# Optimization experiments

Measured on AMD Instinct MI355X. Metric: run time of the kernel, lower is better.

Reference implementation:

```python
import jax, jax.numpy as jnp
import numpy as np

B, L, D, K = 8, 256, 256, 64  # batch, slots, n_input, attn_dimension


def setup_inputs() -> dict:
    key = jax.random.key(0)
    k1, k2, k3 = jax.random.split(key, 3)
    inputs = jax.random.normal(k1, (B, L, D), dtype=jnp.float32)
    # torch.nn.Linear weights are [out_features, in_features]; scale to avoid tanh saturation
    W1 = jax.random.normal(k2, (K, 2 * D), dtype=jnp.float32) * (1.0 / np.sqrt(2 * D))
    W2 = jax.random.normal(k3, (1, K), dtype=jnp.float32) * (1.0 / np.sqrt(K))
    return {"inputs": inputs, "W1": W1, "W2": W2}


def reference(inputs, W1, W2):
    # CONCAT branch of SlotAttention:
    #   score[b,i,j] = W2 @ tanh(W1 @ concat(inputs[b,i], inputs[b,j]))
    # Split W1 into the halves acting on the i-part and j-part of the concat
    # (identical math, avoids materializing the [B,L,L,2D] concat tensor).
    d = inputs.shape[-1]
    W1i, W1j = W1[:, :d], W1[:, d:]
    qi = jnp.einsum('bld,kd->blk', inputs, W1i)          # [B,L,K]
    kj = jnp.einsum('bld,kd->blk', inputs, W1j)          # [B,L,K]
    h = jnp.tanh(qi[:, :, None, :] + kj[:, None, :, :])  # [B,L,L,K]
    scores = jnp.einsum('bijk,k->bij', h, W2[0])         # [B,L,L]
    attn = jax.nn.softmax(scores, axis=2)                # softmax over j
    context = jnp.einsum('bij,bjd->bid', attn, inputs)   # [B,L,D]
    return jnp.concatenate([inputs, context], axis=2)    # [B,L,2D]
```

## Files before the change

### kernel.cpp

```cpp
#include <hip/hip_runtime.h>


#define Bn 8
#define Ln 256
#define Dn 256
#define Kn 64
#define ROWS (Bn*Ln)
#define IPB 4

__global__ __launch_bounds__(128) void proj_kernel(
    const float* __restrict__ X,
    const float* __restrict__ W1,
    float* __restrict__ QK)
{
    __shared__ float Xs[4 * 256];
    const int tid = threadIdx.x;
    const int r0 = blockIdx.x * 4;

    const float4* Xg4 = (const float4*)(X + r0 * Dn);
    float4* Xs4 = (float4*)Xs;
    #pragma unroll
    for (int idx = tid; idx < 256; idx += 128) Xs4[idx] = Xg4[idx];
    __syncthreads();

    const int k = tid & 63, half = tid >> 6;
    const float4* Wrow = (const float4*)(W1 + k * (2 * Dn) + half * Dn);
    float acc[4] = {0, 0, 0, 0};
    #pragma unroll 8
    for (int d4 = 0; d4 < 64; ++d4) {
        float4 w = Wrow[d4];
        #pragma unroll
        for (int r = 0; r < 4; ++r) {
            float4 x = ((const float4*)(Xs + r * Dn))[d4];
            float a = acc[r];
            a = fmaf(w.x, x.x, a);
            a = fmaf(w.y, x.y, a);
            a = fmaf(w.z, x.z, a);
            a = fmaf(w.w, x.w, a);
            acc[r] = a;
        }
    }
    #pragma unroll
    for (int r = 0; r < 4; ++r)
        QK[(r0 + r) * 128 + tid] = __expf(2.0f * acc[r]);
}

__global__ __launch_bounds__(256) void attn_kernel(
    const float* __restrict__ X,
    const float* __restrict__ QK,
    const float* __restrict__ W2,
    float* __restrict__ out)
{
    __shared__ float eq_s[IPB * Kn];
    __shared__ float w2_s[Kn];
    __shared__ float S[Ln * IPB];
    __shared__ float4 red[4 * IPB * 64];

    const int tid = threadIdx.x;
    const int b  = blockIdx.x / (Ln / IPB);
    const int i0 = (blockIdx.x % (Ln / IPB)) * IPB;

    if (tid < Kn) w2_s[tid] = W2[tid];
    {
        int ii = tid >> 6, kk = tid & 63;
        eq_s[ii * Kn + kk] = QK[(b * Ln + i0 + ii) * 128 + kk];
    }

    float ekr[Kn];
    const float4* kj4 = (const float4*)(QK + (b * Ln + tid) * 128 + 64);
    #pragma unroll
    for (int q = 0; q < 16; ++q) {
        float4 v = kj4[q];
        ekr[q * 4 + 0] = v.x; ekr[q * 4 + 1] = v.y;
        ekr[q * 4 + 2] = v.z; ekr[q * 4 + 3] = v.w;
    }
    __syncthreads();

    float s[IPB] = {0, 0, 0, 0};
    const float4* w4  = (const float4*)w2_s;
    const float4* q4a = (const float4*)(eq_s);
    const float4* q4b = (const float4*)(eq_s + Kn);
    const float4* q4c = (const float4*)(eq_s + 2 * Kn);
    const float4* q4d = (const float4*)(eq_s + 3 * Kn);
    #pragma unroll
    for (int k4 = 0; k4 < 16; ++k4) {
        float4 w  = w4[k4];
        float4 q0 = q4a[k4], q1 = q4b[k4], q2 = q4c[k4], q3 = q4d[k4];
        #pragma unroll
        for (int c = 0; c < 4; ++c) {
            float ek = ekr[k4 * 4 + c];
            float wk = (c == 0) ? w.x : (c == 1) ? w.y : (c == 2) ? w.z : w.w;
            float e0 = (c == 0) ? q0.x : (c == 1) ? q0.y : (c == 2) ? q0.z : q0.w;
            float e1 = (c == 0) ? q1.x : (c == 1) ? q1.y : (c == 2) ? q1.z : q1.w;
            float e2 = (c == 0) ? q2.x : (c == 1) ? q2.y : (c == 2) ? q2.z : q2.w;
            float e3 = (c == 0) ? q3.x : (c == 1) ? q3.y : (c == 2) ? q3.z : q3.w;
            s[0] = fmaf(wk, __builtin_amdgcn_rcpf(fmaf(e0, ek, 1.0f)), s[0]);
            s[1] = fmaf(wk, __builtin_amdgcn_rcpf(fmaf(e1, ek, 1.0f)), s[1]);
            s[2] = fmaf(wk, __builtin_amdgcn_rcpf(fmaf(e2, ek, 1.0f)), s[2]);
            s[3] = fmaf(wk, __builtin_amdgcn_rcpf(fmaf(e3, ek, 1.0f)), s[3]);
        }
    }
    ((float4*)S)[tid] = make_float4(s[0], s[1], s[2], s[3]);
    __syncthreads();

    {
        const int wv = tid >> 6, lane = tid & 63;
        float e0 = __expf(-2.0f * S[(lane      ) * IPB + wv]);
        float e1 = __expf(-2.0f * S[(lane +  64) * IPB + wv]);
        float e2 = __expf(-2.0f * S[(lane + 128) * IPB + wv]);
        float e3 = __expf(-2.0f * S[(lane + 192) * IPB + wv]);
        float sum = (e0 + e1) + (e2 + e3);
        #pragma unroll
        for (int off = 32; off > 0; off >>= 1)
            sum += __shfl_xor(sum, off);
        float inv = 1.0f / sum;
        S[(lane      ) * IPB + wv] = e0 * inv;
        S[(lane +  64) * IPB + wv] = e1 * inv;
        S[(lane + 128) * IPB + wv] = e2 * inv;
        S[(lane + 192) * IPB + wv] = e3 * inv;
    }
    __syncthreads();

    {
        const int wv = tid >> 6, lane = tid & 63;
        float4 acc0 = {0,0,0,0}, acc1 = {0,0,0,0}, acc2 = {0,0,0,0}, acc3 = {0,0,0,0};
        const float4* Xb4 = (const float4*)(X + b * Ln * Dn);
        const float4* S4  = (const float4*)S;
        const int jbase = wv * 64;
        #pragma unroll 8
        for (int jj = 0; jj < 64; ++jj) {
            int j = jbase + jj;
            float4 at = S4[j];
            float4 x  = Xb4[j * 64 + lane];
            acc0.x = fmaf(at.x, x.x, acc0.x); acc0.y = fmaf(at.x, x.y, acc0.y);
            acc0.z = fmaf(at.x, x.z, acc0.z); acc0.w = fmaf(at.x, x.w, acc0.w);
            acc1.x = fmaf(at.y, x.x, acc1.x); acc1.y = fmaf(at.y, x.y, acc1.y);
            acc1.z = fmaf(at.y, x.z, acc1.z); acc1.w = fmaf(at.y, x.w, acc1.w);
            acc2.x = fmaf(at.z, x.x, acc2.x); acc2.y = fmaf(at.z, x.y, acc2.y);
            acc2.z = fmaf(at.z, x.z, acc2.z); acc2.w = fmaf(at.z, x.w, acc2.w);
            acc3.x = fmaf(at.w, x.x, acc3.x); acc3.y = fmaf(at.w, x.y, acc3.y);
            acc3.z = fmaf(at.w, x.z, acc3.z); acc3.w = fmaf(at.w, x.w, acc3.w);
        }
        red[(wv * IPB + 0) * 64 + lane] = acc0;
        red[(wv * IPB + 1) * 64 + lane] = acc1;
        red[(wv * IPB + 2) * 64 + lane] = acc2;
        red[(wv * IPB + 3) * 64 + lane] = acc3;
    }
    __syncthreads();

    {
        const int i = tid >> 6, q = tid & 63;
        float4 p0 = red[(0 * IPB + i) * 64 + q];
        float4 p1 = red[(1 * IPB + i) * 64 + q];
        float4 p2 = red[(2 * IPB + i) * 64 + q];
        float4 p3 = red[(3 * IPB + i) * 64 + q];
        float4 c;
        c.x = (p0.x + p1.x) + (p2.x + p3.x);
        c.y = (p0.y + p1.y) + (p2.y + p3.y);
        c.z = (p0.z + p1.z) + (p2.z + p3.z);
        c.w = (p0.w + p1.w) + (p2.w + p3.w);
        const int row = b * Ln + i0 + i;
        float4 xcopy = ((const float4*)(X + row * Dn))[q];
        ((float4*)(out + row * 2 * Dn))[q]      = xcopy;
        ((float4*)(out + row * 2 * Dn + Dn))[q] = c;
    }
}

extern "C" void kernel_launch(void* const* d_in, const int* in_sizes, int n_in,
                              void* d_out, int out_size, void* d_ws, size_t ws_size,
                              hipStream_t stream) {
    const float* X  = (const float*)d_in[0];
    const float* W1 = (const float*)d_in[1];
    const float* W2 = (const float*)d_in[2];
    float* out = (float*)d_out;
    float* QK  = (float*)d_ws;

    proj_kernel<<<ROWS / 4, 128, 0, stream>>>(X, W1, QK);
    attn_kernel<<<ROWS / IPB, 256, 0, stream>>>(X, QK, W2, out);
}
```

Measured before the change: 79.68 us.

## Fuse projection and attention into one cooperative kernel with grid sync

Merges the projection and attention kernels into a single cooperative launch of 512 blocks that use a grid-wide barrier between phases. The query-side exp values stay in shared memory and only the key side goes to the workspace. The X rows are reused from shared memory for the output copy. This removes a kernel launch and the gap between the two kernels, at the cost of a grid sync and the requirement that all 512 blocks be resident at once; the old two-kernel path is kept as a fallback if the cooperative launch fails.

```diff
diff --git a/kernel.cpp b/kernel.cpp
--- a/kernel.cpp
+++ b/kernel.cpp
@@ -1,4 +1,7 @@
 #include <hip/hip_runtime.h>
+#include <hip/hip_cooperative_groups.h>
+
+namespace cg = cooperative_groups;
 
 
 #define Bn 8
@@ -8,96 +11,109 @@
 #define ROWS (Bn*Ln)
 #define IPB 4
 
-__global__ __launch_bounds__(128) void proj_kernel(
+__global__ __launch_bounds__(256, 2) void fused_kernel(
     const float* __restrict__ X,
     const float* __restrict__ W1,
-    float* __restrict__ QK)
-{
-    __shared__ float Xs[4 * 256];
-    const int tid = threadIdx.x;
-    const int r0 = blockIdx.x * 4;
-
-    const float4* Xg4 = (const float4*)(X + r0 * Dn);
-    float4* Xs4 = (float4*)Xs;
-    #pragma unroll
-    for (int idx = tid; idx < 256; idx += 128) Xs4[idx] = Xg4[idx];
-    __syncthreads();
-
-    const int k = tid & 63, half = tid >> 6;
-    const float4* Wrow = (const float4*)(W1 + k * (2 * Dn) + half * Dn);
-    float acc[4] = {0, 0, 0, 0};
-    #pragma unroll 8
-    for (int d4 = 0; d4 < 64; ++d4) {
-        float4 w = Wrow[d4];
-        #pragma unroll
-        for (int r = 0; r < 4; ++r) {
-            float4 x = ((const float4*)(Xs + r * Dn))[d4];
-            float a = acc[r];
-            a = fmaf(w.x, x.x, a);
-            a = fmaf(w.y, x.y, a);
-            a = fmaf(w.z, x.z, a);
-            a = fmaf(w.w, x.w, a);
-            acc[r] = a;
-        }
-    }
-    #pragma unroll
-    for (int r = 0; r < 4; ++r)
-        QK[(r0 + r) * 128 + tid] = __expf(2.0f * acc[r]);
-}
-
-__global__ __launch_bounds__(256) void attn_kernel(
-    const float* __restrict__ X,
-    const float* __restrict__ QK,
     const float* __restrict__ W2,
+    float* __restrict__ QKek,
     float* __restrict__ out)
 {
+    __shared__ float Xs[IPB * Dn];
     __shared__ float eq_s[IPB * Kn];
     __shared__ float w2_s[Kn];
+    __shared__ float pr[128 * 4];
     __shared__ float S[Ln * IPB];
     __shared__ float4 red[4 * IPB * 64];
 
     const int tid = threadIdx.x;
-    const int b  = blockIdx.x / (Ln / IPB);
-    const int i0 = (blockIdx.x % (Ln / IPB)) * IPB;
-
+    const int blk = blockIdx.x;
+    const int r0  = blk * IPB;
+    const int b   = blk >> 6;
+
+    ((float4*)Xs)[tid] = ((const float4*)(X + r0 * Dn))[tid];
     if (tid < Kn) w2_s[tid] = W2[tid];
-    {
-        int ii = tid >> 6, kk = tid & 63;
-        eq_s[ii * Kn + kk] = QK[(b * Ln + i0 + ii) * 128 + kk];
-    }
+    __syncthreads();
+
+    {
+        const int c    = tid & 127;
+        const int dh   = tid >> 7;
+        const int k    = c & 63;
+        const int half = c >> 6;
+        const float4* Wrow = (const float4*)(W1 + k * (2 * Dn) + half * Dn + dh * (Dn / 2));
+        const float4* x0p = (const float4*)(Xs + 0 * Dn + dh * (Dn / 2));
+        const float4* x1p = (const float4*)(Xs + 1 * Dn + dh * (Dn / 2));
+        const float4* x2p = (const float4*)(Xs + 2 * Dn + dh * (Dn / 2));
+        const float4* x3p = (const float4*)(Xs + 3 * Dn + dh * (Dn / 2));
+        float a0 = 0.f, a1 = 0.f, a2 = 0.f, a3 = 0.f;
+        #pragma unroll 8
+        for (int d4 = 0; d4 < 32; ++d4) {
+            float4 w  = Wrow[d4];
+            float4 x0 = x0p[d4], x1 = x1p[d4], x2 = x2p[d4], x3 = x3p[d4];
+            a0 = fmaf(w.x, x0.x, a0); a0 = fmaf(w.y, x0.y, a0);
+            a0 = fmaf(w.z, x0.z, a0); a0 = fmaf(w.w, x0.w, a0);
+            a1 = fmaf(w.x, x1.x, a1); a1 = fmaf(w.y, x1.y, a1);
+            a1 = fmaf(w.z, x1.z, a1); a1 = fmaf(w.w, x1.w, a1);
+            a2 = fmaf(w.x, x2.x, a2); a2 = fmaf(w.y, x2.y, a2);
+            a2 = fmaf(w.z, x2.z, a2); a2 = fmaf(w.w, x2.w, a2);
+            a3 = fmaf(w.x, x3.x, a3); a3 = fmaf(w.y, x3.y, a3);
+            a3 = fmaf(w.z, x3.z, a3); a3 = fmaf(w.w, x3.w, a3);
+        }
+        if (dh) ((float4*)pr)[c] = make_float4(a0, a1, a2, a3);
+        __syncthreads();
+        if (!dh) {
+            float4 p = ((const float4*)pr)[c];
+            float e0 = __expf(2.0f * (a0 + p.x));
+            float e1 = __expf(2.0f * (a1 + p.y));
+            float e2 = __expf(2.0f * (a2 + p.z));
+            float e3 = __expf(2.0f * (a3 + p.w));
+            if (c < Kn) {
+                eq_s[0 * Kn + c] = e0; eq_s[1 * Kn + c] = e1;
+                eq_s[2 * Kn + c] = e2; eq_s[3 * Kn + c] = e3;
+            } else {
+                const int kk = c - Kn;
+                QKek[(r0 + 0) * Kn + kk] = e0; QKek[(r0 + 1) * Kn + kk] = e1;
+                QKek[(r0 + 2) * Kn + kk] = e2; QKek[(r0 + 3) * Kn + kk] = e3;
+            }
+        }
+    }
+
+    cg::this_grid().sync();
 
     float ekr[Kn];
-    const float4* kj4 = (const float4*)(QK + (b * Ln + tid) * 128 + 64);
-    #pragma unroll
-    for (int q = 0; q < 16; ++q) {
-        float4 v = kj4[q];
-        ekr[q * 4 + 0] = v.x; ekr[q * 4 + 1] = v.y;
-        ekr[q * 4 + 2] = v.z; ekr[q * 4 + 3] = v.w;
-    }
-    __syncthreads();
+    {
+        const float4* kj4 = (const float4*)(QKek + (b * Ln + tid) * Kn);
+        #pragma unroll
+        for (int q = 0; q < 16; ++q) {
+            float4 v = kj4[q];
+            ekr[q * 4 + 0] = v.x; ekr[q * 4 + 1] = v.y;
+            ekr[q * 4 + 2] = v.z; ekr[q * 4 + 3] = v.w;
+        }
+    }
 
     float s[IPB] = {0, 0, 0, 0};
-    const float4* w4  = (const float4*)w2_s;
-    const float4* q4a = (const float4*)(eq_s);
-    const float4* q4b = (const float4*)(eq_s + Kn);
-    const float4* q4c = (const float4*)(eq_s + 2 * Kn);
-    const float4* q4d = (const float4*)(eq_s + 3 * Kn);
-    #pragma unroll
-    for (int k4 = 0; k4 < 16; ++k4) {
-        float4 w  = w4[k4];
-        float4 q0 = q4a[k4], q1 = q4b[k4], q2 = q4c[k4], q3 = q4d[k4];
-        #pragma unroll
-        for (int c = 0; c < 4; ++c) {
-            float ek = ekr[k4 * 4 + c];
-            float wk = (c == 0) ? w.x : (c == 1) ? w.y : (c == 2) ? w.z : w.w;
-            float e0 = (c == 0) ? q0.x : (c == 1) ? q0.y : (c == 2) ? q0.z : q0.w;
-            float e1 = (c == 0) ? q1.x : (c == 1) ? q1.y : (c == 2) ? q1.z : q1.w;
-            float e2 = (c == 0) ? q2.x : (c == 1) ? q2.y : (c == 2) ? q2.z : q2.w;
-            float e3 = (c == 0) ? q3.x : (c == 1) ? q3.y : (c == 2) ? q3.z : q3.w;
-            s[0] = fmaf(wk, __builtin_amdgcn_rcpf(fmaf(e0, ek, 1.0f)), s[0]);
-            s[1] = fmaf(wk, __builtin_amdgcn_rcpf(fmaf(e1, ek, 1.0f)), s[1]);
-            s[2] = fmaf(wk, __builtin_amdgcn_rcpf(fmaf(e2, ek, 1.0f)), s[2]);
-            s[3] = fmaf(wk, __builtin_amdgcn_rcpf(fmaf(e3, ek, 1.0f)), s[3]);
+    {
+        const float4* w4  = (const float4*)w2_s;
+        const float4* q4a = (const float4*)(eq_s);
+        const float4* q4b = (const float4*)(eq_s + Kn);
+        const float4* q4c = (const float4*)(eq_s + 2 * Kn);
+        const float4* q4d = (const float4*)(eq_s + 3 * Kn);
+        #pragma unroll
+        for (int k4 = 0; k4 < 16; ++k4) {
+            float4 w  = w4[k4];
+            float4 q0 = q4a[k4], q1 = q4b[k4], q2 = q4c[k4], q3 = q4d[k4];
+            #pragma unroll
+            for (int c = 0; c < 4; ++c) {
+                float ek = ekr[k4 * 4 + c];
+                float wk = (c == 0) ? w.x : (c == 1) ? w.y : (c == 2) ? w.z : w.w;
+                float e0 = (c == 0) ? q0.x : (c == 1) ? q0.y : (c == 2) ? q0.z : q0.w;
+                float e1 = (c == 0) ? q1.x : (c == 1) ? q1.y : (c == 2) ? q1.z : q1.w;
+                float e2 = (c == 0) ? q2.x : (c == 1) ? q2.y : (c == 2) ? q2.z : q2.w;
+                float e3 = (c == 0) ? q3.x : (c == 1) ? q3.y : (c == 2) ? q3.z : q3.w;
+                s[0] = fmaf(wk, __builtin_amdgcn_rcpf(fmaf(e0, ek, 1.0f)), s[0]);
+                s[1] = fmaf(wk, __builtin_amdgcn_rcpf(fmaf(e1, ek, 1.0f)), s[1]);
+                s[2] = fmaf(wk, __builtin_amdgcn_rcpf(fmaf(e2, ek, 1.0f)), s[2]);
+                s[3] = fmaf(wk, __builtin_amdgcn_rcpf(fmaf(e3, ek, 1.0f)), s[3]);
+            }
         }
     }
     ((float4*)S)[tid] = make_float4(s[0], s[1], s[2], s[3]);
@@ -159,6 +175,149 @@
         c.y = (p0.y + p1.y) + (p2.y + p3.y);
         c.z = (p0.z + p1.z) + (p2.z + p3.z);
         c.w = (p0.w + p1.w) + (p2.w + p3.w);
+        const int row = r0 + i;
+        float4 xcopy = ((const float4*)(Xs + i * Dn))[q];
+        ((float4*)(out + row * 2 * Dn))[q]      = xcopy;
+        ((float4*)(out + row * 2 * Dn + Dn))[q] = c;
+    }
+}
+
+__global__ __launch_bounds__(128) void proj_kernel(
+    const float* __restrict__ X, const float* __restrict__ W1, float* __restrict__ QK)
+{
+    __shared__ float Xs[4 * 256];
+    const int tid = threadIdx.x;
+    const int r0 = blockIdx.x * 4;
+    const float4* Xg4 = (const float4*)(X + r0 * Dn);
+    float4* Xs4 = (float4*)Xs;
+    #pragma unroll
+    for (int idx = tid; idx < 256; idx += 128) Xs4[idx] = Xg4[idx];
+    __syncthreads();
+    const int k = tid & 63, half = tid >> 6;
+    const float4* Wrow = (const float4*)(W1 + k * (2 * Dn) + half * Dn);
+    float acc[4] = {0, 0, 0, 0};
+    #pragma unroll 8
+    for (int d4 = 0; d4 < 64; ++d4) {
+        float4 w = Wrow[d4];
+        #pragma unroll
+        for (int r = 0; r < 4; ++r) {
+            float4 x = ((const float4*)(Xs + r * Dn))[d4];
+            float a = acc[r];
+            a = fmaf(w.x, x.x, a); a = fmaf(w.y, x.y, a);
+            a = fmaf(w.z, x.z, a); a = fmaf(w.w, x.w, a);
+            acc[r] = a;
+        }
+    }
+    #pragma unroll
+    for (int r = 0; r < 4; ++r)
+        QK[(r0 + r) * 128 + tid] = __expf(2.0f * acc[r]);
+}
+
+__global__ __launch_bounds__(256) void attn_kernel(
+    const float* __restrict__ X, const float* __restrict__ QK,
+    const float* __restrict__ W2, float* __restrict__ out)
+{
+    __shared__ float eq_s[IPB * Kn];
+    __shared__ float w2_s[Kn];
+    __shared__ float S[Ln * IPB];
+    __shared__ float4 red[4 * IPB * 64];
+    const int tid = threadIdx.x;
+    const int b  = blockIdx.x / (Ln / IPB);
+    const int i0 = (blockIdx.x % (Ln / IPB)) * IPB;
+    if (tid < Kn) w2_s[tid] = W2[tid];
+    {
+        int ii = tid >> 6, kk = tid & 63;
+        eq_s[ii * Kn + kk] = QK[(b * Ln + i0 + ii) * 128 + kk];
+    }
+    float ekr[Kn];
+    const float4* kj4 = (const float4*)(QK + (b * Ln + tid) * 128 + 64);
+    #pragma unroll
+    for (int q = 0; q < 16; ++q) {
+        float4 v = kj4[q];
+        ekr[q * 4 + 0] = v.x; ekr[q * 4 + 1] = v.y;
+        ekr[q * 4 + 2] = v.z; ekr[q * 4 + 3] = v.w;
+    }
+    __syncthreads();
+    float s[IPB] = {0, 0, 0, 0};
+    const float4* w4  = (const float4*)w2_s;
+    const float4* q4a = (const float4*)(eq_s);
+    const float4* q4b = (const float4*)(eq_s + Kn);
+    const float4* q4c = (const float4*)(eq_s + 2 * Kn);
+    const float4* q4d = (const float4*)(eq_s + 3 * Kn);
+    #pragma unroll
+    for (int k4 = 0; k4 < 16; ++k4) {
+        float4 w  = w4[k4];
+        float4 q0 = q4a[k4], q1 = q4b[k4], q2 = q4c[k4], q3 = q4d[k4];
+        #pragma unroll
+        for (int c = 0; c < 4; ++c) {
+            float ek = ekr[k4 * 4 + c];
+            float wk = (c == 0) ? w.x : (c == 1) ? w.y : (c == 2) ? w.z : w.w;
+            float e0 = (c == 0) ? q0.x : (c == 1) ? q0.y : (c == 2) ? q0.z : q0.w;
+            float e1 = (c == 0) ? q1.x : (c == 1) ? q1.y : (c == 2) ? q1.z : q1.w;
+            float e2 = (c == 0) ? q2.x : (c == 1) ? q2.y : (c == 2) ? q2.z : q2.w;
+            float e3 = (c == 0) ? q3.x : (c == 1) ? q3.y : (c == 2) ? q3.z : q3.w;
+            s[0] = fmaf(wk, __builtin_amdgcn_rcpf(fmaf(e0, ek, 1.0f)), s[0]);
+            s[1] = fmaf(wk, __builtin_amdgcn_rcpf(fmaf(e1, ek, 1.0f)), s[1]);
+            s[2] = fmaf(wk, __builtin_amdgcn_rcpf(fmaf(e2, ek, 1.0f)), s[2]);
+            s[3] = fmaf(wk, __builtin_amdgcn_rcpf(fmaf(e3, ek, 1.0f)), s[3]);
+        }
+    }
+    ((float4*)S)[tid] = make_float4(s[0], s[1], s[2], s[3]);
+    __syncthreads();
+    {
+        const int wv = tid >> 6, lane = tid & 63;
+        float e0 = __expf(-2.0f * S[(lane      ) * IPB + wv]);
+        float e1 = __expf(-2.0f * S[(lane +  64) * IPB + wv]);
+        float e2 = __expf(-2.0f * S[(lane + 128) * IPB + wv]);
+        float e3 = __expf(-2.0f * S[(lane + 192) * IPB + wv]);
+        float sum = (e0 + e1) + (e2 + e3);
+        #pragma unroll
+        for (int off = 32; off > 0; off >>= 1)
+            sum += __shfl_xor(sum, off);
+        float inv = 1.0f / sum;
+        S[(lane      ) * IPB + wv] = e0 * inv;
+        S[(lane +  64) * IPB + wv] = e1 * inv;
+        S[(lane + 128) * IPB + wv] = e2 * inv;
+        S[(lane + 192) * IPB + wv] = e3 * inv;
+    }
+    __syncthreads();
+    {
+        const int wv = tid >> 6, lane = tid & 63;
+        float4 acc0 = {0,0,0,0}, acc1 = {0,0,0,0}, acc2 = {0,0,0,0}, acc3 = {0,0,0,0};
+        const float4* Xb4 = (const float4*)(X + b * Ln * Dn);
+        const float4* S4  = (const float4*)S;
+        const int jbase = wv * 64;
+        #pragma unroll 8
+        for (int jj = 0; jj < 64; ++jj) {
+            int j = jbase + jj;
+            float4 at = S4[j];
+            float4 x  = Xb4[j * 64 + lane];
+            acc0.x = fmaf(at.x, x.x, acc0.x); acc0.y = fmaf(at.x, x.y, acc0.y);
+            acc0.z = fmaf(at.x, x.z, acc0.z); acc0.w = fmaf(at.x, x.w, acc0.w);
+            acc1.x = fmaf(at.y, x.x, acc1.x); acc1.y = fmaf(at.y, x.y, acc1.y);
+            acc1.z = fmaf(at.y, x.z, acc1.z); acc1.w = fmaf(at.y, x.w, acc1.w);
+            acc2.x = fmaf(at.z, x.x, acc2.x); acc2.y = fmaf(at.z, x.y, acc2.y);
+            acc2.z = fmaf(at.z, x.z, acc2.z); acc2.w = fmaf(at.z, x.w, acc2.w);
+            acc3.x = fmaf(at.w, x.x, acc3.x); acc3.y = fmaf(at.w, x.y, acc3.y);
+            acc3.z = fmaf(at.w, x.z, acc3.z); acc3.w = fmaf(at.w, x.w, acc3.w);
+        }
+        red[(wv * IPB + 0) * 64 + lane] = acc0;
+        red[(wv * IPB + 1) * 64 + lane] = acc1;
+        red[(wv * IPB + 2) * 64 + lane] = acc2;
+        red[(wv * IPB + 3) * 64 + lane] = acc3;
+    }
+    __syncthreads();
+    {
+        const int i = tid >> 6, q = tid & 63;
+        float4 p0 = red[(0 * IPB + i) * 64 + q];
+        float4 p1 = red[(1 * IPB + i) * 64 + q];
+        float4 p2 = red[(2 * IPB + i) * 64 + q];
+        float4 p3 = red[(3 * IPB + i) * 64 + q];
+        float4 c;
+        c.x = (p0.x + p1.x) + (p2.x + p3.x);
+        c.y = (p0.y + p1.y) + (p2.y + p3.y);
+        c.z = (p0.z + p1.z) + (p2.z + p3.z);
+        c.w = (p0.w + p1.w) + (p2.w + p3.w);
         const int row = b * Ln + i0 + i;
         float4 xcopy = ((const float4*)(X + row * Dn))[q];
         ((float4*)(out + row * 2 * Dn))[q]      = xcopy;
@@ -173,8 +332,14 @@
     const float* W1 = (const float*)d_in[1];
     const float* W2 = (const float*)d_in[2];
     float* out = (float*)d_out;
-    float* QK  = (float*)d_ws;
-
-    proj_kernel<<<ROWS / 4, 128, 0, stream>>>(X, W1, QK);
-    attn_kernel<<<ROWS / IPB, 256, 0, stream>>>(X, QK, W2, out);
+    float* ws  = (float*)d_ws;
+
+    void* args[] = {(void*)&X, (void*)&W1, (void*)&W2, (void*)&ws, (void*)&out};
+    hipError_t err = hipLaunchCooperativeKernel((const void*)fused_kernel,
+                                                dim3(ROWS / IPB), dim3(256),
+                                                args, 0, stream);
+    if (err != hipSuccess) {
+        proj_kernel<<<ROWS / 4, 128, 0, stream>>>(X, W1, ws);
+        attn_kernel<<<ROWS / IPB, 256, 0, stream>>>(X, ws, W2, out);
+    }
 }
```

Measured after the change: 134.6 us. +68.9%, slower.

## Double rows per block, transpose key exps, split K across threads, restructure context GEMV

Applied to the files above, without the earlier changes.

Each attention block now handles 8 query rows with 512 threads. The K dimension is split into two halves across thread groups, and the partial scores are combined in shared memory before the softmax. The projection kernel stages W1 through a swizzled shared-memory tile and writes the key exponentials transposed (k-major), so attention threads can load them with coalesced scalar reads. The context stage drops the cross-wave reduction: each thread accumulates one output column over all 256 j for 4 rows. This doubles reuse of each key vector and each X tile per block, at the cost of fewer blocks, more registers per thread and extra workspace.

```diff
diff --git a/kernel.cpp b/kernel.cpp
--- a/kernel.cpp
+++ b/kernel.cpp
@@ -6,46 +6,58 @@
 #define Dn 256
 #define Kn 64
 #define ROWS (Bn*Ln)
-#define IPB 4
+#define IPB 8
+#define EKT_BASE (ROWS*128)
 
-__global__ __launch_bounds__(128) void proj_kernel(
+__global__ __launch_bounds__(512) void proj_kernel(
     const float* __restrict__ X,
     const float* __restrict__ W1,
     float* __restrict__ QK)
 {
-    __shared__ float Xs[4 * 256];
+    __shared__ float Xs[IPB * Dn];
+    __shared__ float Wl[Kn * 128];
     const int tid = threadIdx.x;
-    const int r0 = blockIdx.x * 4;
+    const int r0 = blockIdx.x * IPB;
 
-    const float4* Xg4 = (const float4*)(X + r0 * Dn);
-    float4* Xs4 = (float4*)Xs;
+    ((float4*)Xs)[tid] = ((const float4*)(X + r0 * Dn))[tid];
+
+    const int k = tid & 63;
+    const int r = tid >> 6;
+    float accI = 0.f, accJ = 0.f;
+
     #pragma unroll
-    for (int idx = tid; idx < 256; idx += 128) Xs4[idx] = Xg4[idx];
-    __syncthreads();
-
-    const int k = tid & 63, half = tid >> 6;
-    const float4* Wrow = (const float4*)(W1 + k * (2 * Dn) + half * Dn);
-    float acc[4] = {0, 0, 0, 0};
-    #pragma unroll 8
-    for (int d4 = 0; d4 < 64; ++d4) {
-        float4 w = Wrow[d4];
+    for (int h = 0; h < 2; ++h) {
         #pragma unroll
-        for (int r = 0; r < 4; ++r) {
-            float4 x = ((const float4*)(Xs + r * Dn))[d4];
-            float a = acc[r];
-            a = fmaf(w.x, x.x, a);
-            a = fmaf(w.y, x.y, a);
-            a = fmaf(w.z, x.z, a);
-            a = fmaf(w.w, x.w, a);
-            acc[r] = a;
+        for (int ds = 0; ds < 2; ++ds) {
+            __syncthreads();
+            #pragma unroll
+            for (int t = 0; t < 4; ++t) {
+                int f  = tid + t * 512;
+                int kk = f >> 5, c4 = f & 31;
+                float4 w = *(const float4*)(W1 + kk * (2 * Dn) + h * Dn + ds * 128 + c4 * 4);
+                ((float4*)Wl)[kk * 32 + (c4 ^ (kk & 31))] = w;
+            }
+            __syncthreads();
+            float a = 0.f;
+            const float4* xrow = (const float4*)(Xs + r * Dn + ds * 128);
+            #pragma unroll
+            for (int c4 = 0; c4 < 32; ++c4) {
+                float4 w = ((const float4*)Wl)[k * 32 + (c4 ^ (k & 31))];
+                float4 x = xrow[c4];
+                a = fmaf(w.x, x.x, a); a = fmaf(w.y, x.y, a);
+                a = fmaf(w.z, x.z, a); a = fmaf(w.w, x.w, a);
+            }
+            if (h == 0) accI += a; else accJ += a;
         }
     }
-    #pragma unroll
-    for (int r = 0; r < 4; ++r)
-        QK[(r0 + r) * 128 + tid] = __expf(2.0f * acc[r]);
+
+    const int row = r0 + r;
+    QK[row * 128 + k] = __expf(2.0f * accI);
+    const int bb = row >> 8, jj = row & 255;
+    QK[EKT_BASE + bb * (Kn * Ln) + k * Ln + jj] = __expf(2.0f * accJ);
 }
 
-__global__ __launch_bounds__(256) void attn_kernel(
+__global__ __launch_bounds__(512) void attn_kernel(
     const float* __restrict__ X,
     const float* __restrict__ QK,
     const float* __restrict__ W2,
@@ -53,116 +65,100 @@
 {
     __shared__ float eq_s[IPB * Kn];
     __shared__ float w2_s[Kn];
-    __shared__ float S[Ln * IPB];
-    __shared__ float4 red[4 * IPB * 64];
+    __shared__ float Sp[2 * IPB * Ln];
+    __shared__ float S8[Ln * IPB];
 
     const int tid = threadIdx.x;
-    const int b  = blockIdx.x / (Ln / IPB);
-    const int i0 = (blockIdx.x % (Ln / IPB)) * IPB;
+    const int b  = blockIdx.x >> 5;
+    const int i0 = (blockIdx.x & 31) * IPB;
+    const int j  = tid & 255;
+    const int kh = tid >> 8;
 
     if (tid < Kn) w2_s[tid] = W2[tid];
+    eq_s[tid] = QK[(b * Ln + i0 + (tid >> 6)) * 128 + (tid & 63)];
+
+    float ekr[32];
     {
-        int ii = tid >> 6, kk = tid & 63;
-        eq_s[ii * Kn + kk] = QK[(b * Ln + i0 + ii) * 128 + kk];
-    }
-
-    float ekr[Kn];
-    const float4* kj4 = (const float4*)(QK + (b * Ln + tid) * 128 + 64);
-    #pragma unroll
-    for (int q = 0; q < 16; ++q) {
-        float4 v = kj4[q];
-        ekr[q * 4 + 0] = v.x; ekr[q * 4 + 1] = v.y;
-        ekr[q * 4 + 2] = v.z; ekr[q * 4 + 3] = v.w;
+        const float* ekt = QK + EKT_BASE + b * (Kn * Ln) + (kh * 32) * Ln + j;
+        #pragma unroll
+        for (int kk = 0; kk < 32; ++kk) ekr[kk] = ekt[kk * Ln];
     }
     __syncthreads();
 
-    float s[IPB] = {0, 0, 0, 0};
-    const float4* w4  = (const float4*)w2_s;
-    const float4* q4a = (const float4*)(eq_s);
-    const float4* q4b = (const float4*)(eq_s + Kn);
-    const float4* q4c = (const float4*)(eq_s + 2 * Kn);
-    const float4* q4d = (const float4*)(eq_s + 3 * Kn);
-    #pragma unroll
-    for (int k4 = 0; k4 < 16; ++k4) {
-        float4 w  = w4[k4];
-        float4 q0 = q4a[k4], q1 = q4b[k4], q2 = q4c[k4], q3 = q4d[k4];
+    {
+        float s[IPB] = {0, 0, 0, 0, 0, 0, 0, 0};
+        const float4* w4 = ((const float4*)w2_s) + kh * 8;
         #pragma unroll
-        for (int c = 0; c < 4; ++c) {
-            float ek = ekr[k4 * 4 + c];
-            float wk = (c == 0) ? w.x : (c == 1) ? w.y : (c == 2) ? w.z : w.w;
-            float e0 = (c == 0) ? q0.x : (c == 1) ? q0.y : (c == 2) ? q0.z : q0.w;
-            float e1 = (c == 0) ? q1.x : (c == 1) ? q1.y : (c == 2) ? q1.z : q1.w;
-            float e2 = (c == 0) ? q2.x : (c == 1) ? q2.y : (c == 2) ? q2.z : q2.w;
-            float e3 = (c == 0) ? q3.x : (c == 1) ? q3.y : (c == 2) ? q3.z : q3.w;
-            s[0] = fmaf(wk, __builtin_amdgcn_rcpf(fmaf(e0, ek, 1.0f)), s[0]);
-            s[1] = fmaf(wk, __builtin_amdgcn_rcpf(fmaf(e1, ek, 1.0f)), s[1]);
-            s[2] = fmaf(wk, __builtin_amdgcn_rcpf(fmaf(e2, ek, 1.0f)), s[2]);
-            s[3] = fmaf(wk, __builtin_amdgcn_rcpf(fmaf(e3, ek, 1.0f)), s[3]);
+        for (int k4 = 0; k4 < 8; ++k4) {
+            float4 w = w4[k4];
+            float4 q[IPB];
+            #pragma unroll
+            for (int i = 0; i < IPB; ++i)
+                q[i] = ((const float4*)(eq_s + i * Kn))[kh * 8 + k4];
+            #pragma unroll
+            for (int c = 0; c < 4; ++c) {
+                float ek = ekr[k4 * 4 + c];
+                float wk = (c == 0) ? w.x : (c == 1) ? w.y : (c == 2) ? w.z : w.w;
+                #pragma unroll
+                for (int i = 0; i < IPB; ++i) {
+                    float e = (c == 0) ? q[i].x : (c == 1) ? q[i].y
+                            : (c == 2) ? q[i].z : q[i].w;
+                    s[i] = fmaf(wk, __builtin_amdgcn_rcpf(fmaf(e, ek, 1.0f)), s[i]);
+                }
+            }
         }
+        #pragma unroll
+        for (int i = 0; i < IPB; ++i)
+            Sp[(kh * IPB + i) * Ln + j] = s[i];
     }
-    ((float4*)S)[tid] = make_float4(s[0], s[1], s[2], s[3]);
     __syncthreads();
 
     {
         const int wv = tid >> 6, lane = tid & 63;
-        float e0 = __expf(-2.0f * S[(lane      ) * IPB + wv]);
-        float e1 = __expf(-2.0f * S[(lane +  64) * IPB + wv]);
-        float e2 = __expf(-2.0f * S[(lane + 128) * IPB + wv]);
-        float e3 = __expf(-2.0f * S[(lane + 192) * IPB + wv]);
+        const float* p0 = Sp + wv * Ln;
+        const float* p1 = Sp + (IPB + wv) * Ln;
+        float e0 = __expf(-2.0f * (p0[lane      ] + p1[lane      ]));
+        float e1 = __expf(-2.0f * (p0[lane +  64] + p1[lane +  64]));
+        float e2 = __expf(-2.0f * (p0[lane + 128] + p1[lane + 128]));
+        float e3 = __expf(-2.0f * (p0[lane + 192] + p1[lane + 192]));
         float sum = (e0 + e1) + (e2 + e3);
         #pragma unroll
         for (int off = 32; off > 0; off >>= 1)
             sum += __shfl_xor(sum, off);
         float inv = 1.0f / sum;
-        S[(lane      ) * IPB + wv] = e0 * inv;
-        S[(lane +  64) * IPB + wv] = e1 * inv;
-        S[(lane + 128) * IPB + wv] = e2 * inv;
-        S[(lane + 192) * IPB + wv] = e3 * inv;
-    }
-    __syncthreads();
-
-    {
-        const int wv = tid >> 6, lane = tid & 63;
-        float4 acc0 = {0,0,0,0}, acc1 = {0,0,0,0}, acc2 = {0,0,0,0}, acc3 = {0,0,0,0};
-        const float4* Xb4 = (const float4*)(X + b * Ln * Dn);
-        const float4* S4  = (const float4*)S;
-        const int jbase = wv * 64;
-        #pragma unroll 8
-        for (int jj = 0; jj < 64; ++jj) {
-            int j = jbase + jj;
-            float4 at = S4[j];
-            float4 x  = Xb4[j * 64 + lane];
-            acc0.x = fmaf(at.x, x.x, acc0.x); acc0.y = fmaf(at.x, x.y, acc0.y);
-            acc0.z = fmaf(at.x, x.z, acc0.z); acc0.w = fmaf(at.x, x.w, acc0.w);
-            acc1.x = fmaf(at.y, x.x, acc1.x); acc1.y = fmaf(at.y, x.y, acc1.y);
-            acc1.z = fmaf(at.y, x.z, acc1.z); acc1.w = fmaf(at.y, x.w, acc1.w);
-            acc2.x = fmaf(at.z, x.x, acc2.x); acc2.y = fmaf(at.z, x.y, acc2.y);
-            acc2.z = fmaf(at.z, x.z, acc2.z); acc2.w = fmaf(at.z, x.w, acc2.w);
-            acc3.x = fmaf(at.w, x.x, acc3.x); acc3.y = fmaf(at.w, x.y, acc3.y);
-            acc3.z = fmaf(at.w, x.z, acc3.z); acc3.w = fmaf(at.w, x.w, acc3.w);
-        }
-        red[(wv * IPB + 0) * 64 + lane] = acc0;
-        red[(wv * IPB + 1) * 64 + lane] = acc1;
-        red[(wv * IPB + 2) * 64 + lane] = acc2;
-        red[(wv * IPB + 3) * 64 + lane] = acc3;
+        S8[(lane      ) * IPB + wv] = e0 * inv;
+        S8[(lane +  64) * IPB + wv] = e1 * inv;
+        S8[(lane + 128) * IPB + wv] = e2 * inv;
+        S8[(lane + 192) * IPB + wv] = e3 * inv;
     }
     __syncthreads();
 
     {
         const int i = tid >> 6, q = tid & 63;
-        float4 p0 = red[(0 * IPB + i) * 64 + q];
-        float4 p1 = red[(1 * IPB + i) * 64 + q];
-        float4 p2 = red[(2 * IPB + i) * 64 + q];
-        float4 p3 = red[(3 * IPB + i) * 64 + q];
-        float4 c;
-        c.x = (p0.x + p1.x) + (p2.x + p3.x);
-        c.y = (p0.y + p1.y) + (p2.y + p3.y);
-        c.z = (p0.z + p1.z) + (p2.z + p3.z);
-        c.w = (p0.w + p1.w) + (p2.w + p3.w);
         const int row = b * Ln + i0 + i;
-        float4 xcopy = ((const float4*)(X + row * Dn))[q];
-        ((float4*)(out + row * 2 * Dn))[q]      = xcopy;
-        ((float4*)(out + row * 2 * Dn + Dn))[q] = c;
+        ((float4*)(out + row * 2 * Dn))[q] = ((const float4*)(X + row * Dn))[q];
+    }
+
+    {
+        const int wv = tid >> 6, lane = tid & 63;
+        const int rq = wv >> 2, dh = wv & 3;
+        const int d  = dh * 64 + lane;
+        const float* Xb = X + b * Ln * Dn + d;
+        float a0 = 0.f, a1 = 0.f, a2 = 0.f, a3 = 0.f;
+        #pragma unroll 8
+        for (int jj = 0; jj < Ln; ++jj) {
+            float4 at = *(const float4*)(S8 + jj * IPB + rq * 4);
+            float xv = Xb[jj * Dn];
+            a0 = fmaf(at.x, xv, a0);
+            a1 = fmaf(at.y, xv, a1);
+            a2 = fmaf(at.z, xv, a2);
+            a3 = fmaf(at.w, xv, a3);
+        }
+        const int row0 = b * Ln + i0 + rq * 4;
+        out[(row0 + 0) * 2 * Dn + Dn + d] = a0;
+        out[(row0 + 1) * 2 * Dn + Dn + d] = a1;
+        out[(row0 + 2) * 2 * Dn + Dn + d] = a2;
+        out[(row0 + 3) * 2 * Dn + Dn + d] = a3;
     }
 }
 
@@ -175,6 +171,6 @@
     float* out = (float*)d_out;
     float* QK  = (float*)d_ws;
 
-    proj_kernel<<<ROWS / 4, 128, 0, stream>>>(X, W1, QK);
-    attn_kernel<<<ROWS / IPB, 256, 0, stream>>>(X, QK, W2, out);
+    proj_kernel<<<ROWS / IPB, 512, 0, stream>>>(X, W1, QK);
+    attn_kernel<<<ROWS / IPB, 512, 0, stream>>>(X, QK, W2, out);
 }
```

Measured after the change: 82.24 us. 1.03x slower.
